# Kernel tuning notes

Hardware: AMD Instinct MI355X
Metric: run time of the kernel (lower is better)

The kernel has to match this reference:

```python
import jax, jax.numpy as jnp
import numpy as np

B, S, D, E = 2, 2048, 1024, 16  # batch, cutoff (seq), dmodel, n_experts


def setup_inputs() -> dict:
    key = jax.random.key(0)
    k = jax.random.split(key, 6)
    scale = 1.0 / np.sqrt(D)
    return {
        "x": jax.random.normal(k[0], (B, S, D), dtype=jnp.float32),
        "gate": jax.random.normal(k[1], (D, E), dtype=jnp.float32) * scale,
        "W1": jax.random.normal(k[2], (E, D, D), dtype=jnp.float32) * scale,  # lin1: Linear(dmodel, dmodel*E), split per expert
        "b1": jnp.zeros((E, D), dtype=jnp.float32),
        "W2": jax.random.normal(k[3], (E, D, D), dtype=jnp.float32) * scale,  # lin2: Linear(dmodel*E, dmodel), split per expert
        "b2": jnp.zeros((D,), dtype=jnp.float32),
        "topk": 256,
    }


def reference(x, gate, W1, b1, W2, b2, topk):
    # Expert-choice gating: softmax over the token (cutoff) axis per expert.
    logits = jnp.einsum("bsd,de->bse", x, gate)            # (B, S, E)
    probs = jax.nn.softmax(logits, axis=1)                  # softmax over tokens
    # Each expert selects its top-k tokens.
    g, idx = jax.lax.top_k(jnp.swapaxes(probs, 1, 2), topk)  # (B, E, k)
    # Gather selected tokens: (B, E, k, D)
    xin = jnp.take_along_axis(x[:, None, :, :], idx[..., None], axis=2)
    # Per-expert 2-layer FFN (hidden size = dmodel, per width = dmodel*n_experts)
    h = jax.nn.relu(jnp.einsum("bekd,edf->bekf", xin, W1) + b1[None, :, None, :])
    out = jnp.einsum("bekf,efd->bekd", h, W2) + b2           # (B, E, k, D)
    weighted = out * g[..., None]
    # Scatter-add back to token positions.
    y = jnp.zeros_like(x)
    b_idx = jnp.arange(x.shape[0])[:, None, None]            # (B, 1, 1)
    y = y.at[b_idx, idx].add(weighted)
    return y
```

## Files before the change

kernel.cpp:

```cpp
#include <hip/hip_runtime.h>
#include <stdint.h>
#include <math.h>

constexpr int CB = 2;
constexpr int CS = 2048;
constexpr int CD = 1024;
constexpr int CE = 16;
constexpr int CK = 256;

typedef short bf16x8 __attribute__((ext_vector_type(8)));
typedef float f32x4 __attribute__((ext_vector_type(4)));

__device__ inline unsigned short f2bf(float f) {
    union { float f; uint32_t u; } v; v.f = f;
    uint32_t u = v.u;
    uint32_t r = (u + 0x7FFFu + ((u >> 16) & 1u)) >> 16;
    return (unsigned short)r;
}

__global__ void logits_kernel(const float* __restrict__ x,
                              const float* __restrict__ gate,
                              float* __restrict__ logits) {
    const int bs = blockIdx.x;
    const int l = threadIdx.x;
    const float* xr = x + (size_t)bs * CD;
    float acc[CE];
#pragma unroll
    for (int e = 0; e < CE; e++) acc[e] = 0.0f;
    for (int i = 0; i < CD / 64; i++) {
        const int d = i * 64 + l;
        const float xv = xr[d];
        const float* g = gate + (size_t)d * CE;
#pragma unroll
        for (int e = 0; e < CE; e++) acc[e] += xv * g[e];
    }
#pragma unroll
    for (int e = 0; e < CE; e++) {
        float v = acc[e];
#pragma unroll
        for (int o = 32; o > 0; o >>= 1) v += __shfl_down(v, o);
        if (l == 0) logits[(size_t)bs * CE + e] = v;
    }
}

__global__ void topk_kernel(const float* __restrict__ logits,
                            int* __restrict__ idx_out,
                            float* __restrict__ g_out) {
    const int be = blockIdx.x;
    const int b = be >> 4, e = be & 15;
    const int tid = threadIdx.x;
    const int lane = tid & 63, wid = tid >> 6;

    __shared__ float redf[4];
    __shared__ int redi[4];
    __shared__ int scnt, eqc;
    __shared__ int eqbuf[CS];

    float lv[8], p[8];
    unsigned int uv[8];
#pragma unroll
    for (int j = 0; j < 8; j++) {
        const int s = tid + j * 256;
        lv[j] = logits[((size_t)(b * CS + s)) * CE + e];
    }
    float m = lv[0];
#pragma unroll
    for (int j = 1; j < 8; j++) m = fmaxf(m, lv[j]);
#pragma unroll
    for (int o = 32; o > 0; o >>= 1) m = fmaxf(m, __shfl_down(m, o));
    if (lane == 0) redf[wid] = m;
    __syncthreads();
    m = fmaxf(fmaxf(redf[0], redf[1]), fmaxf(redf[2], redf[3]));
    __syncthreads();
    float lsum = 0.0f;
#pragma unroll
    for (int j = 0; j < 8; j++) {
        p[j] = expf(lv[j] - m);
        uv[j] = __float_as_uint(p[j]);
        lsum += p[j];
    }
#pragma unroll
    for (int o = 32; o > 0; o >>= 1) lsum += __shfl_down(lsum, o);
    if (lane == 0) redf[wid] = lsum;
    __syncthreads();
    const float total = redf[0] + redf[1] + redf[2] + redf[3];
    const float inv_total = 1.0f / total;
    __syncthreads();

    unsigned int lo = 0u, hi = 0xFFFFFFFFu;
    while (lo < hi) {
        const unsigned int mid = lo + ((hi - lo) >> 1) + 1u;
        int c = 0;
#pragma unroll
        for (int j = 0; j < 8; j++) c += (uv[j] >= mid) ? 1 : 0;
#pragma unroll
        for (int o = 32; o > 0; o >>= 1) c += __shfl_down(c, o);
        if (lane == 0) redi[wid] = c;
        __syncthreads();
        c = redi[0] + redi[1] + redi[2] + redi[3];
        __syncthreads();
        if (c >= CK) lo = mid; else hi = mid - 1u;
    }
    const unsigned int v = lo;

    if (tid == 0) { scnt = 0; eqc = 0; }
    __syncthreads();
#pragma unroll
    for (int j = 0; j < 8; j++) {
        const int s = tid + j * 256;
        if (uv[j] > v) {
            const int pos = atomicAdd(&scnt, 1);
            idx_out[be * CK + pos] = s;
            g_out[be * CK + pos] = p[j] * inv_total;
        } else if (uv[j] == v) {
            const int pos = atomicAdd(&eqc, 1);
            eqbuf[pos] = s;
        }
    }
    __syncthreads();
    if (tid == 0) {
        const int cgt = scnt;
        const int quota = CK - cgt;
        const int n = eqc;
        const float gv = __uint_as_float(v) * inv_total;
        if (n > quota) {
            for (int i = 0; i < quota; i++) {
                int mn = i;
                for (int k2 = i + 1; k2 < n; k2++)
                    if (eqbuf[k2] < eqbuf[mn]) mn = k2;
                const int t2 = eqbuf[i]; eqbuf[i] = eqbuf[mn]; eqbuf[mn] = t2;
            }
        }
        for (int i = 0; i < quota; i++) {
            idx_out[be * CK + cgt + i] = eqbuf[i];
            g_out[be * CK + cgt + i] = gv;
        }
    }
}

__global__ void gather_kernel(const float* __restrict__ x,
                              const int* __restrict__ idx_ws,
                              unsigned short* __restrict__ xinbuf) {
    const int row = blockIdx.x;
    const int be = row >> 8;
    const int b = be >> 4;
    const int tok = idx_ws[row];
    const int c0 = threadIdx.x * 4;
    const f32x4 f = *(const f32x4*)(x + ((size_t)b * CS + tok) * CD + c0);
    union { unsigned short u[4]; uint2 v; } t;
    t.u[0] = f2bf(f[0]); t.u[1] = f2bf(f[1]); t.u[2] = f2bf(f[2]); t.u[3] = f2bf(f[3]);
    *(uint2*)(xinbuf + (size_t)row * CD + c0) = t.v;
}

template <int PHASE>
__global__ __launch_bounds__(256, 2)
void ffn_gemm(const unsigned short* __restrict__ Ain,
              const float* __restrict__ W,
              const float* __restrict__ bias,
              unsigned short* __restrict__ hout,
              const int* __restrict__ idx_ws,
              const float* __restrict__ g_ws,
              float* __restrict__ y) {
    const int mtile = blockIdx.x;
    const int ntile = blockIdx.y;
    const int be = blockIdx.z;
    const int b = be >> 4, e = be & 15;
    const int tid = threadIdx.x;
    const int w = tid >> 6, l = tid & 63;
    const int wm = w & 1, wn = w >> 1;
    const int quad = l >> 4, lr = l & 15;

    __shared__ __align__(16) unsigned short As[128 * 40];
    __shared__ __align__(16) unsigned short Bs[128 * 40];

    f32x4 acc[4][4];
    const f32x4 zz = {0.f, 0.f, 0.f, 0.f};
#pragma unroll
    for (int mi = 0; mi < 4; mi++)
#pragma unroll
        for (int ni = 0; ni < 4; ni++) acc[mi][ni] = zz;

    const int arow = tid >> 2;
    const int acol = (tid & 3) << 3;
    const unsigned short* aptr[2];
#pragma unroll
    for (int p = 0; p < 2; p++)
        aptr[p] = Ain + ((size_t)be * CK + mtile * 128 + p * 64 + arow) * CD + acol;

    const int bn = tid & 127;
    const int bh = tid >> 7;
    const float* wsrc = W + (size_t)e * CD * CD + (size_t)(bh * 16) * CD + ntile * 128 + bn;

    for (int ks = 0; ks < CD / 32; ks++) {
        const int k0 = ks * 32;
#pragma unroll
        for (int p = 0; p < 2; p++) {
            union { unsigned short u[8]; uint4 v; } t;
            t.v = *(const uint4*)(aptr[p] + k0);
            *(uint4*)(&As[(p * 64 + arow) * 40 + acol]) = t.v;
        }
        {
            union { unsigned short u[16]; uint4 v[2]; } t;
            const float* s0 = wsrc + (size_t)k0 * CD;
#pragma unroll
            for (int kk = 0; kk < 16; kk++) t.u[kk] = f2bf(s0[(size_t)kk * CD]);
            *(uint4*)(&Bs[bn * 40 + bh * 16]) = t.v[0];
            *(uint4*)(&Bs[bn * 40 + bh * 16 + 8]) = t.v[1];
        }
        __syncthreads();

        bf16x8 af[4], bf[4];
#pragma unroll
        for (int mi = 0; mi < 4; mi++)
            af[mi] = *(const bf16x8*)&As[(wm * 64 + mi * 16 + lr) * 40 + quad * 8];
#pragma unroll
        for (int ni = 0; ni < 4; ni++)
            bf[ni] = *(const bf16x8*)&Bs[(wn * 64 + ni * 16 + lr) * 40 + quad * 8];
#pragma unroll
        for (int mi = 0; mi < 4; mi++)
#pragma unroll
            for (int ni = 0; ni < 4; ni++)
                acc[mi][ni] = __builtin_amdgcn_mfma_f32_16x16x32_bf16(
                    af[mi], bf[ni], acc[mi][ni], 0, 0, 0);
        __syncthreads();
    }

    const int gn_base = ntile * 128 + wn * 64;
    if (PHASE == 0) {
#pragma unroll
        for (int mi = 0; mi < 4; mi++)
#pragma unroll
            for (int r = 0; r < 4; r++) {
                const int slot = mtile * 128 + wm * 64 + mi * 16 + quad * 4 + r;
                unsigned short* outrow = hout + ((size_t)be * CK + slot) * CD;
#pragma unroll
                for (int ni = 0; ni < 4; ni++) {
                    const int col = gn_base + ni * 16 + lr;
                    float hv = acc[mi][ni][r] + bias[e * CD + col];
                    hv = fmaxf(hv, 0.0f);
                    outrow[col] = f2bf(hv);
                }
            }
    } else {
#pragma unroll
        for (int mi = 0; mi < 4; mi++)
#pragma unroll
            for (int r = 0; r < 4; r++) {
                const int slot = mtile * 128 + wm * 64 + mi * 16 + quad * 4 + r;
                const int tok = idx_ws[be * CK + slot];
                const float gval = g_ws[be * CK + slot];
                float* yrow = y + ((size_t)b * CS + tok) * CD;
#pragma unroll
                for (int ni = 0; ni < 4; ni++) {
                    const int col = gn_base + ni * 16 + lr;
                    const float val = (acc[mi][ni][r] + bias[col]) * gval;
                    atomicAdd(&yrow[col], val);
                }
            }
    }
}

extern "C" void kernel_launch(void* const* d_in, const int* in_sizes, int n_in,
                              void* d_out, int out_size, void* d_ws, size_t ws_size,
                              hipStream_t stream) {
    const float* x    = (const float*)d_in[0];
    const float* gate = (const float*)d_in[1];
    const float* W1   = (const float*)d_in[2];
    const float* b1   = (const float*)d_in[3];
    const float* W2   = (const float*)d_in[4];
    const float* b2   = (const float*)d_in[5];
    float* y = (float*)d_out;

    char* ws = (char*)d_ws;
    float* logits = (float*)ws;
    int* idxw = (int*)(ws + 262144);
    float* gw = (float*)(ws + 262144 + 32768);
    unsigned short* xinbuf = (unsigned short*)(ws + 262144 + 65536);
    unsigned short* hbuf = (unsigned short*)(ws + 262144 + 65536 + (size_t)CB * CE * CK * CD * 2);

    logits_kernel<<<CB * CS, 64, 0, stream>>>(x, gate, logits);
    topk_kernel<<<CB * CE, 256, 0, stream>>>(logits, idxw, gw);
    gather_kernel<<<CB * CE * CK, 256, 0, stream>>>(x, idxw, xinbuf);
    hipMemsetAsync(d_out, 0, (size_t)CB * CS * CD * sizeof(float), stream);
    ffn_gemm<0><<<dim3(2, 8, CB * CE), 256, 0, stream>>>(xinbuf, W1, b1, hbuf, idxw, gw, y);
    ffn_gemm<1><<<dim3(2, 8, CB * CE), 256, 0, stream>>>(hbuf, W2, b2, nullptr, idxw, gw, y);
}
```

Before: 309.8 us.

## Pre-transpose weights to bf16, use async LDS loads, radix-select top-k

Adds a kernel that converts each expert's fp32 weight matrix into a transposed bf16 copy before each GEMM. The GEMM then streams both operands with 16-byte global-to-LDS async loads instead of strided fp32 column reads with per-element conversion. The top-k threshold search is replaced by a 4-pass 8-bit radix histogram select, and the grid is reordered so both batches of the same expert run adjacently for weight reuse in cache. This adds two transform launches and extra workspace traffic, and drops the LDS padding, which may introduce bank conflicts.

```diff
diff --git a/kernel.cpp b/kernel.cpp
--- a/kernel.cpp
+++ b/kernel.cpp
@@ -10,6 +10,13 @@
 
 typedef short bf16x8 __attribute__((ext_vector_type(8)));
 typedef float f32x4 __attribute__((ext_vector_type(4)));
+
+typedef __attribute__((address_space(1))) const unsigned int gu32;
+typedef __attribute__((address_space(3))) unsigned int lu32;
+
+__device__ __forceinline__ void async16(const void* g, void* l) {
+    __builtin_amdgcn_global_load_lds((gu32*)g, (lu32*)l, 16, 0, 0);
+}
 
 __device__ inline unsigned short f2bf(float f) {
     union { float f; uint32_t u; } v; v.f = f;
@@ -52,7 +59,9 @@
     const int lane = tid & 63, wid = tid >> 6;
 
     __shared__ float redf[4];
-    __shared__ int redi[4];
+    __shared__ int hist[256];
+    __shared__ int wsum[4];
+    __shared__ int sh_bin, sh_rank;
     __shared__ int scnt, eqc;
     __shared__ int eqbuf[CS];
 
@@ -85,23 +94,42 @@
     __syncthreads();
     const float total = redf[0] + redf[1] + redf[2] + redf[3];
     const float inv_total = 1.0f / total;
-    __syncthreads();
-
-    unsigned int lo = 0u, hi = 0xFFFFFFFFu;
-    while (lo < hi) {
-        const unsigned int mid = lo + ((hi - lo) >> 1) + 1u;
-        int c = 0;
-#pragma unroll
-        for (int j = 0; j < 8; j++) c += (uv[j] >= mid) ? 1 : 0;
-#pragma unroll
-        for (int o = 32; o > 0; o >>= 1) c += __shfl_down(c, o);
-        if (lane == 0) redi[wid] = c;
-        __syncthreads();
-        c = redi[0] + redi[1] + redi[2] + redi[3];
-        __syncthreads();
-        if (c >= CK) lo = mid; else hi = mid - 1u;
-    }
-    const unsigned int v = lo;
+
+    unsigned int prefix = 0;
+    int kneed = CK;
+    for (int pass = 0; pass < 4; pass++) {
+        const int shift = 24 - 8 * pass;
+        __syncthreads();
+        hist[tid] = 0;
+        __syncthreads();
+        const unsigned int hmask = (pass == 0) ? 0u : (0xFFFFFFFFu << (shift + 8));
+#pragma unroll
+        for (int j = 0; j < 8; j++)
+            if ((uv[j] & hmask) == prefix)
+                atomicAdd(&hist[(uv[j] >> shift) & 255], 1);
+        __syncthreads();
+        const int own = hist[tid];
+        int s = own;
+#pragma unroll
+        for (int o = 1; o < 64; o <<= 1) {
+            int t = __shfl_down(s, o);
+            if (lane + o < 64) s += t;
+        }
+        if (lane == 0) wsum[wid] = s;
+        __syncthreads();
+        int above = 0;
+        for (int ww = wid + 1; ww < 4; ww++) above += wsum[ww];
+        const int incl = s + above;
+        if (incl >= kneed && (incl - own) < kneed) {
+            sh_bin = tid;
+            sh_rank = kneed - (incl - own);
+        }
+        __syncthreads();
+        prefix |= ((unsigned int)sh_bin) << shift;
+        kneed = sh_rank;
+    }
+    const unsigned int v = prefix;
+    const int quota = kneed;
 
     if (tid == 0) { scnt = 0; eqc = 0; }
     __syncthreads();
@@ -120,7 +148,6 @@
     __syncthreads();
     if (tid == 0) {
         const int cgt = scnt;
-        const int quota = CK - cgt;
         const int n = eqc;
         const float gv = __uint_as_float(v) * inv_total;
         if (n > quota) {
@@ -152,10 +179,43 @@
     *(uint2*)(xinbuf + (size_t)row * CD + c0) = t.v;
 }
 
+__global__ __launch_bounds__(256)
+void wt_kernel(const float* __restrict__ W, unsigned short* __restrict__ Wt) {
+    const int kt = blockIdx.x, nt = blockIdx.y, e = blockIdx.z;
+    const float* src = W + (size_t)e * CD * CD;
+    unsigned short* dst = Wt + (size_t)e * CD * CD;
+    const int tid = threadIdx.x;
+    __shared__ unsigned short T[64 * 64];
+
+    const int kr = tid >> 4;
+    const int n4 = (tid & 15) << 2;
+#pragma unroll
+    for (int it = 0; it < 4; it++) {
+        const int k = it * 16 + kr;
+        const f32x4 v = *(const f32x4*)(src + (size_t)(kt * 64 + k) * CD + nt * 64 + n4);
+        const int pp = k >> 4;
+        const int klo = k & 15;
+#pragma unroll
+        for (int i = 0; i < 4; i++) {
+            const int n = n4 + i;
+            T[n * 64 + ((pp ^ ((n >> 2) & 3)) << 4) + klo] = f2bf(v[i]);
+        }
+    }
+    __syncthreads();
+    const int n = tid >> 2;
+    const int pp = tid & 3;
+    const int sw = pp ^ ((n >> 2) & 3);
+    const uint4 a = *(const uint4*)&T[n * 64 + (sw << 4)];
+    const uint4 b = *(const uint4*)&T[n * 64 + (sw << 4) + 8];
+    unsigned short* drow = dst + (size_t)(nt * 64 + n) * CD + kt * 64 + pp * 16;
+    *(uint4*)drow = a;
+    *(uint4*)(drow + 8) = b;
+}
+
 template <int PHASE>
 __global__ __launch_bounds__(256, 2)
 void ffn_gemm(const unsigned short* __restrict__ Ain,
-              const float* __restrict__ W,
+              const unsigned short* __restrict__ Wt,
               const float* __restrict__ bias,
               unsigned short* __restrict__ hout,
               const int* __restrict__ idx_ws,
@@ -163,15 +223,16 @@
               float* __restrict__ y) {
     const int mtile = blockIdx.x;
     const int ntile = blockIdx.y;
-    const int be = blockIdx.z;
-    const int b = be >> 4, e = be & 15;
+    const int z = blockIdx.z;
+    const int e = z >> 1, b = z & 1;
+    const int be = b * 16 + e;
     const int tid = threadIdx.x;
     const int w = tid >> 6, l = tid & 63;
     const int wm = w & 1, wn = w >> 1;
     const int quad = l >> 4, lr = l & 15;
 
-    __shared__ __align__(16) unsigned short As[128 * 40];
-    __shared__ __align__(16) unsigned short Bs[128 * 40];
+    __shared__ __align__(16) unsigned short As[128 * 32];
+    __shared__ __align__(16) unsigned short Bs[128 * 32];
 
     f32x4 acc[4][4];
     const f32x4 zz = {0.f, 0.f, 0.f, 0.f};
@@ -180,42 +241,29 @@
 #pragma unroll
         for (int ni = 0; ni < 4; ni++) acc[mi][ni] = zz;
 
-    const int arow = tid >> 2;
-    const int acol = (tid & 3) << 3;
-    const unsigned short* aptr[2];
-#pragma unroll
-    for (int p = 0; p < 2; p++)
-        aptr[p] = Ain + ((size_t)be * CK + mtile * 128 + p * 64 + arow) * CD + acol;
-
-    const int bn = tid & 127;
-    const int bh = tid >> 7;
-    const float* wsrc = W + (size_t)e * CD * CD + (size_t)(bh * 16) * CD + ntile * 128 + bn;
-
-    for (int ks = 0; ks < CD / 32; ks++) {
-        const int k0 = ks * 32;
-#pragma unroll
-        for (int p = 0; p < 2; p++) {
-            union { unsigned short u[8]; uint4 v; } t;
-            t.v = *(const uint4*)(aptr[p] + k0);
-            *(uint4*)(&As[(p * 64 + arow) * 40 + acol]) = t.v;
-        }
-        {
-            union { unsigned short u[16]; uint4 v[2]; } t;
-            const float* s0 = wsrc + (size_t)k0 * CD;
-#pragma unroll
-            for (int kk = 0; kk < 16; kk++) t.u[kk] = f2bf(s0[(size_t)kk * CD]);
-            *(uint4*)(&Bs[bn * 40 + bh * 16]) = t.v[0];
-            *(uint4*)(&Bs[bn * 40 + bh * 16 + 8]) = t.v[1];
+    const int sr = l >> 2;
+    const int sc = l & 3;
+    const unsigned short* Abase = Ain + ((size_t)be * CK + mtile * 128) * CD;
+    const unsigned short* Bbase = Wt + ((size_t)e * CD + ntile * 128) * CD;
+
+    for (int k0 = 0; k0 < CD; k0 += 32) {
+#pragma unroll
+        for (int j = 0; j < 2; j++) {
+            const int row = (w * 2 + j) * 16 + sr;
+            const size_t goff = (size_t)row * CD + k0 + sc * 8;
+            const int loff = (w * 2 + j) * 512 + l * 8;
+            async16(Abase + goff, &As[loff]);
+            async16(Bbase + goff, &Bs[loff]);
         }
         __syncthreads();
 
         bf16x8 af[4], bf[4];
 #pragma unroll
         for (int mi = 0; mi < 4; mi++)
-            af[mi] = *(const bf16x8*)&As[(wm * 64 + mi * 16 + lr) * 40 + quad * 8];
+            af[mi] = *(const bf16x8*)&As[(wm * 64 + mi * 16 + lr) * 32 + quad * 8];
 #pragma unroll
         for (int ni = 0; ni < 4; ni++)
-            bf[ni] = *(const bf16x8*)&Bs[(wn * 64 + ni * 16 + lr) * 40 + quad * 8];
+            bf[ni] = *(const bf16x8*)&Bs[(wn * 64 + ni * 16 + lr) * 32 + quad * 8];
 #pragma unroll
         for (int mi = 0; mi < 4; mi++)
 #pragma unroll
@@ -274,14 +322,17 @@
     char* ws = (char*)d_ws;
     float* logits = (float*)ws;
     int* idxw = (int*)(ws + 262144);
-    float* gw = (float*)(ws + 262144 + 32768);
-    unsigned short* xinbuf = (unsigned short*)(ws + 262144 + 65536);
-    unsigned short* hbuf = (unsigned short*)(ws + 262144 + 65536 + (size_t)CB * CE * CK * CD * 2);
+    float* gw = (float*)(ws + 294912);
+    unsigned short* xinbuf = (unsigned short*)(ws + 327680);
+    unsigned short* hbuf = (unsigned short*)(ws + 17104896);
+    unsigned short* wtbuf = (unsigned short*)(ws + 33882112);
 
     logits_kernel<<<CB * CS, 64, 0, stream>>>(x, gate, logits);
     topk_kernel<<<CB * CE, 256, 0, stream>>>(logits, idxw, gw);
     gather_kernel<<<CB * CE * CK, 256, 0, stream>>>(x, idxw, xinbuf);
+    wt_kernel<<<dim3(16, 16, CE), 256, 0, stream>>>(W1, wtbuf);
     hipMemsetAsync(d_out, 0, (size_t)CB * CS * CD * sizeof(float), stream);
-    ffn_gemm<0><<<dim3(2, 8, CB * CE), 256, 0, stream>>>(xinbuf, W1, b1, hbuf, idxw, gw, y);
-    ffn_gemm<1><<<dim3(2, 8, CB * CE), 256, 0, stream>>>(hbuf, W2, b2, nullptr, idxw, gw, y);
-}
+    ffn_gemm<0><<<dim3(2, 8, CB * CE), 256, 0, stream>>>(xinbuf, wtbuf, b1, hbuf, idxw, gw, y);
+    wt_kernel<<<dim3(16, 16, CE), 256, 0, stream>>>(W2, wtbuf);
+    ffn_gemm<1><<<dim3(2, 8, CB * CE), 256, 0, stream>>>(hbuf, wtbuf, b2, nullptr, idxw, gw, y);
+}
```

After: 302.8 us. 1.02x faster.
